# Optimization experiments

Hardware: AMD Instinct MI355X
Metric: run time of the kernel (lower is better)

The kernel has to match this reference:

```python
import jax, jax.numpy as jnp
import numpy as np

E = 1024
H = 16
DH = E // H
EPS = 1e-8
GRAM_W = 1.5


def _gram_scores(q, k1, k2):
    # q: [BH, L, D], k1/k2: [BH, S, D] -> [BH, L, S]
    ll = jnp.sum(q * q, -1)[:, :, None]          # [BH, L, 1]
    vv = jnp.sum(k1 * k1, -1)[:, None, :]        # [BH, 1, S]
    aa = jnp.sum(k2 * k2, -1)[:, None, :]
    va = jnp.sum(k1 * k2, -1)[:, None, :]
    lv = jnp.einsum('bld,bsd->bls', q, k1)
    la = jnp.einsum('bld,bsd->bls', q, k2)
    det = ll * (vv * aa - va * va) - lv * (lv * aa - la * va) + la * (lv * va - la * vv)
    return -jnp.sqrt(jnp.clip(det, EPS, None))


def setup_inputs() -> dict:
    key = jax.random.key(0)
    ks = jax.random.split(key, 20)
    L, B, S = 512, 4, 1024
    inp = {
        'query': jax.random.normal(ks[0], (L, B, E), jnp.float32),
        'mod1': jax.random.normal(ks[1], (S, B, E), jnp.float32),
        'mod2': jax.random.normal(ks[2], (S, B, E), jnp.float32),
    }
    # Linear params stored as [in, out] (y = x @ W + b), 8 linears
    names = ['q', 'k1', 'k2', 'v1', 'v2', 'g1', 'g2', 'o']
    for i, n in enumerate(names):
        inp[n + '_w'] = jax.random.normal(ks[3 + 2 * i], (E, E), jnp.float32) * 0.02
        inp[n + '_b'] = jax.random.normal(ks[4 + 2 * i], (E,), jnp.float32) * 0.02
    return inp


def reference(query, mod1, mod2,
              q_w, q_b, k1_w, k1_b, k2_w, k2_b, v1_w, v1_b, v2_w, v2_b,
              g1_w, g1_b, g2_w, g2_b, o_w, o_b):
    L, B, _ = query.shape
    S = mod1.shape[0]
    scaling = DH ** -0.5

    def lin(x, w, b):
        return x @ w + b

    def split_heads(x, n):  # [n, B, E] -> [B*H, n, DH]
        return x.reshape(n, B * H, DH).transpose(1, 0, 2)

    q = split_heads(lin(query, q_w, q_b) * scaling, L)
    k1 = split_heads(lin(mod1, k1_w, k1_b), S)
    k2 = split_heads(lin(mod2, k2_w, k2_b), S)
    v1 = split_heads(lin(mod1, v1_w, v1_b), S)
    v2 = split_heads(lin(mod2, v2_w, v2_b), S)

    w1 = jnp.einsum('bld,bsd->bls', q, k1)
    w2 = jnp.einsum('bld,bsd->bls', q, k2)
    gram = _gram_scores(q, k1, k2)
    logits = GRAM_W * gram + w1 + w2          # [BH, L, S]
    attn = jax.nn.softmax(logits, axis=-1)

    def merge_heads(x):  # [B*H, L, DH] -> [L, B, E]
        return x.transpose(1, 0, 2).reshape(L, B, E)

    out1 = merge_heads(jnp.einsum('bls,bsd->bld', attn, v1))
    out2 = merge_heads(jnp.einsum('bls,bsd->bld', attn, v2))
    gate1 = jax.nn.sigmoid(lin(query, g1_w, g1_b))
    gate2 = jax.nn.sigmoid(lin(query, g2_w, g2_b))
    attn_output = lin((out1 * gate1 + out2 * gate2) / 2.0, o_w, o_b)
    avg_weights = attn.reshape(B, H, L, S).mean(axis=1)
    return attn_output, avg_weights
```

## Files before the change

kernel.cpp:

```cpp
#include <hip/hip_runtime.h>
#include <cstddef>
#include <cstdint>

typedef unsigned short ushort_t;
typedef unsigned int uint_t;
typedef __attribute__((ext_vector_type(8))) short short8;
typedef __attribute__((ext_vector_type(4))) float f32x4;

#define EDIM 1024
#define NHEAD 16
#define HDIM 64
#define NB 4
#define LQ 512
#define SK 1024
#define BHD 64

__device__ __forceinline__ ushort_t f2b(float f) {
    uint_t u = __float_as_uint(f);
    return (ushort_t)((u + 0x7fffu + ((u >> 16) & 1u)) >> 16);
}
__device__ __forceinline__ float b2f(ushort_t b) {
    return __uint_as_float(((uint_t)b) << 16);
}

__device__ __forceinline__ void gload_lds16(const void* g, void* l) {
    __builtin_amdgcn_global_load_lds((const __attribute__((address_space(1))) void*)g,
                                     (__attribute__((address_space(3))) void*)l, 16, 0, 0);
}

struct MegaArgs {
    const ushort_t *qx, *m1h, *m1l, *m2h, *m2l;
    const ushort_t *Wqg, *Wkv1, *Wkv2, *Wk1l, *Wk2l;
    const float *q_b, *k1_b, *k2_b, *v1_b, *v2_b, *g1_b, *g2_b;
    float *K1f, *K2f;
    ushort_t *V1b, *V2b, *Qb, *G1b, *G2b;
};

__global__ __launch_bounds__(256, 2)
void mega_gemm(MegaArgs a)
{
    __shared__ ushort_t As[128 * 64];
    __shared__ ushort_t Bs[128 * 64];
    const int tid = threadIdx.x;
    const int wave = tid >> 6, lane = tid & 63;
    const int ln = lane & 15, lq = lane >> 4;
    const int wm = wave & 1, wn = wave >> 1;
    const int mrl = lane >> 3;
    const int lswz = (lane & 7) ^ mrl;

    const int id = blockIdx.x;
    f32x4 zero = {0.f, 0.f, 0.f, 0.f};

    if (id < 512) {
        const int kind = id >> 8;
        const int t = id & 255;
        const int u = t >> 3;
        const int col0 = (u >> 2) * 128;
        const int row0 = ((t & 7) * 4 + (u & 3)) * 128;
        const ushort_t* Ah  = kind ? a.m2h : a.m1h;
        const ushort_t* Alo = kind ? a.m2l : a.m1l;
        const ushort_t* Bh  = kind ? a.Wkv2 : a.Wkv1;
        const ushort_t* Blo = kind ? a.Wk2l : a.Wk1l;
        const float* bias = kind ? a.k2_b : a.k1_b;

        f32x4 acc[4][4];
#pragma unroll
        for (int i = 0; i < 4; ++i)
#pragma unroll
            for (int j = 0; j < 4; ++j) acc[i][j] = zero;

        const int ksub = (lswz & 3) * 8;
        const ushort_t* Asrc = (lswz & 4) ? Alo : Ah;
        const ushort_t* Bsrc = (lswz & 4) ? Blo : Bh;

        for (int kk = 0; kk < 1024; kk += 32) {
            __syncthreads();
#pragma unroll
            for (int j = 0; j < 4; ++j) {
                const int mr = (wave * 4 + j) * 8 + mrl;
                gload_lds16(Asrc + (size_t)(row0 + mr) * 1024 + kk + ksub,
                            (void*)(As + (wave * 4 + j) * 512));
                gload_lds16(Bsrc + (size_t)(col0 + mr) * 1024 + kk + ksub,
                            (void*)(Bs + (wave * 4 + j) * 512));
            }
            __syncthreads();
            short8 ah[4], alv[4], bh[4], blv[4];
#pragma unroll
            for (int i = 0; i < 4; ++i) {
                const int ml = wm * 64 + i * 16 + ln;
                const int pa = (lq ^ (ml & 7)) * 8;
                ah[i]  = *(const short8*)(As + ml * 64 + pa);
                alv[i] = *(const short8*)(As + ml * 64 + (pa ^ 32));
                const int nl = wn * 64 + i * 16 + ln;
                const int pb = (lq ^ (nl & 7)) * 8;
                bh[i]  = *(const short8*)(Bs + nl * 64 + pb);
                blv[i] = *(const short8*)(Bs + nl * 64 + (pb ^ 32));
            }
#pragma unroll
            for (int i = 0; i < 4; ++i)
#pragma unroll
                for (int j = 0; j < 4; ++j)
                    acc[i][j] = __builtin_amdgcn_mfma_f32_16x16x32_bf16(ah[i], bh[j], acc[i][j], 0, 0, 0);
#pragma unroll
            for (int i = 0; i < 4; ++i)
#pragma unroll
                for (int j = 0; j < 4; ++j)
                    acc[i][j] = __builtin_amdgcn_mfma_f32_16x16x32_bf16(ah[i], blv[j], acc[i][j], 0, 0, 0);
#pragma unroll
            for (int i = 0; i < 4; ++i)
#pragma unroll
                for (int j = 0; j < 4; ++j)
                    acc[i][j] = __builtin_amdgcn_mfma_f32_16x16x32_bf16(alv[i], bh[j], acc[i][j], 0, 0, 0);
        }

        float* Y = kind ? a.K2f : a.K1f;
#pragma unroll
        for (int i = 0; i < 4; ++i) {
#pragma unroll
            for (int r = 0; r < 4; ++r) {
                const int row = row0 + wm * 64 + i * 16 + lq * 4 + r;
#pragma unroll
                for (int j = 0; j < 4; ++j) {
                    const int col = col0 + wn * 64 + j * 16 + ln;
                    const float v = acc[i][j][r] + bias[col];
                    const int s = row >> 2, b = row & 3, h = col >> 6, d = col & 63;
                    Y[(((size_t)(b * 16 + h)) * 1024 + s) * 64 + d] = v;
                }
            }
        }
        return;
    }

    int kind, row0, col0;
    const ushort_t *A, *B;
    const float* bias;
    if (id < 1024) {
        int t = id - 512; kind = 2 + (t >> 8); t &= 255;
        const int u = t >> 3;
        col0 = (u >> 2) * 128;
        row0 = ((t & 7) * 4 + (u & 3)) * 128;
        A = (kind == 2) ? a.m1h : a.m2h;
        B = ((kind == 2) ? a.Wkv1 : a.Wkv2) + (size_t)1024 * 1024;
        bias = (kind == 2) ? a.v1_b : a.v2_b;
    } else {
        const int t = id - 1024; kind = 4;
        const int u = t >> 3;
        const int c = (t & 7) * 3 + (u >> 4);
        const int rr = u & 15;
        col0 = c * 128; row0 = rr * 128;
        A = a.qx; B = a.Wqg;
        const int seg = c >> 3;
        bias = (seg == 0) ? a.q_b : ((seg == 1) ? a.g1_b : a.g2_b);
    }

    f32x4 acc[4][4];
#pragma unroll
    for (int i = 0; i < 4; ++i)
#pragma unroll
        for (int j = 0; j < 4; ++j) acc[i][j] = zero;

    for (int kk = 0; kk < 1024; kk += 64) {
        __syncthreads();
#pragma unroll
        for (int j = 0; j < 4; ++j) {
            const int mr = (wave * 4 + j) * 8 + mrl;
            gload_lds16(A + (size_t)(row0 + mr) * 1024 + kk + lswz * 8,
                        (void*)(As + (wave * 4 + j) * 512));
            gload_lds16(B + (size_t)(col0 + mr) * 1024 + kk + lswz * 8,
                        (void*)(Bs + (wave * 4 + j) * 512));
        }
        __syncthreads();
#pragma unroll
        for (int sub = 0; sub < 2; ++sub) {
            short8 af[4], bfv[4];
#pragma unroll
            for (int i = 0; i < 4; ++i) {
                const int ml = wm * 64 + i * 16 + ln;
                af[i] = *(const short8*)(As + ml * 64 + (((sub * 4 + lq) ^ (ml & 7)) * 8));
                const int nl = wn * 64 + i * 16 + ln;
                bfv[i] = *(const short8*)(Bs + nl * 64 + (((sub * 4 + lq) ^ (nl & 7)) * 8));
            }
#pragma unroll
            for (int i = 0; i < 4; ++i)
#pragma unroll
                for (int j = 0; j < 4; ++j)
                    acc[i][j] = __builtin_amdgcn_mfma_f32_16x16x32_bf16(af[i], bfv[j], acc[i][j], 0, 0, 0);
        }
    }

#pragma unroll
    for (int i = 0; i < 4; ++i) {
#pragma unroll
        for (int r = 0; r < 4; ++r) {
            const int row = row0 + wm * 64 + i * 16 + lq * 4 + r;
#pragma unroll
            for (int j = 0; j < 4; ++j) {
                const int col = col0 + wn * 64 + j * 16 + ln;
                const int lc = col & 1023;
                float v = acc[i][j][r] + bias[lc];
                if (kind <= 3) {
                    const int s = row >> 2, b = row & 3, h = lc >> 6, d = lc & 63;
                    ushort_t* Y = (kind == 2) ? a.V1b : a.V2b;
                    Y[(((size_t)(b * 16 + h)) * 1024 + s) * 64 + d] = f2b(v);
                } else {
                    const int seg = col >> 10;
                    if (seg == 0) {
                        v *= 0.125f;
                        const int s = row >> 2, b = row & 3, h = lc >> 6, d = lc & 63;
                        a.Qb[(((size_t)(b * 16 + h)) * 512 + s) * 64 + d] = f2b(v);
                    } else {
                        v = 1.0f / (1.0f + __expf(-v));
                        ushort_t* Y = (seg == 1) ? a.G1b : a.G2b;
                        Y[(size_t)row * 1024 + lc] = f2b(v);
                    }
                }
            }
        }
    }
}

struct CastArgs {
    const float* q; const float* m1; const float* m2;
    ushort_t* qx; ushort_t* m1h; ushort_t* m1l; ushort_t* m2h; ushort_t* m2l;
    const float* wsrc[8];
    ushort_t* whi[8];
    ushort_t* wlo[8];
};

__global__ __launch_bounds__(256)
void casts_kernel(CastArgs a)
{
    __shared__ float T[64][65];
    const int id = blockIdx.x;
    const int tid = threadIdx.x;
    if (id < 1024) {
        const size_t i = ((size_t)id * 256 + tid) * 8;
        float4 x = *(const float4*)(a.q + i);
        float4 y = *(const float4*)(a.q + i + 4);
        ushort_t o[8] = {f2b(x.x), f2b(x.y), f2b(x.z), f2b(x.w), f2b(y.x), f2b(y.y), f2b(y.z), f2b(y.w)};
        *(uint4*)( (void*)(a.qx + i) ) = *(const uint4*)o;
    } else if (id < 5120) {
        const int t = id - 1024;
        const int which = t >> 11;
        const float* x = which ? a.m2 : a.m1;
        ushort_t* yh = which ? a.m2h : a.m1h;
        ushort_t* yl = which ? a.m2l : a.m1l;
        const size_t i = ((size_t)(t & 2047) * 256 + tid) * 8;
        float v[8];
        *(float4*)v = *(const float4*)(x + i);
        *(float4*)(v + 4) = *(const float4*)(x + i + 4);
        ushort_t oh[8], ol[8];
#pragma unroll
        for (int k = 0; k < 8; ++k) {
            oh[k] = f2b(v[k]);
            ol[k] = f2b(v[k] - b2f(oh[k]));
        }
        *(uint4*)( (void*)(yh + i) ) = *(const uint4*)oh;
        *(uint4*)( (void*)(yl + i) ) = *(const uint4*)ol;
    } else {
        const int t = id - 5120;
        const int z = t >> 8, x = t & 15, y = (t >> 4) & 15;
        const float* W = a.wsrc[z];
        ushort_t* Th = a.whi[z];
        ushort_t* Tl = a.wlo[z];
        const int k0 = x * 64, n0 = y * 64;
        const int r = tid >> 2, cg = (tid & 3) * 16;
#pragma unroll
        for (int u = 0; u < 4; ++u) {
            float4 v = *(const float4*)(W + (size_t)(k0 + r) * 1024 + n0 + cg + u * 4);
            T[r][cg + u * 4 + 0] = v.x; T[r][cg + u * 4 + 1] = v.y;
            T[r][cg + u * 4 + 2] = v.z; T[r][cg + u * 4 + 3] = v.w;
        }
        __syncthreads();
        ushort_t oh[16], ol[16];
#pragma unroll
        for (int u = 0; u < 16; ++u) {
            float v = T[cg + u][r];
            oh[u] = f2b(v);
            ol[u] = f2b(v - b2f(oh[u]));
        }
        ushort_t* dh = Th + (size_t)(n0 + r) * 1024 + k0 + cg;
        *(uint4*)( (void*)dh ) = *(const uint4*)oh;
        *(uint4*)( (void*)(dh + 8) ) = *(const uint4*)(oh + 8);
        if (Tl) {
            ushort_t* dl = Tl + (size_t)(n0 + r) * 1024 + k0 + cg;
            *(uint4*)( (void*)dl ) = *(const uint4*)ol;
            *(uint4*)( (void*)(dl + 8) ) = *(const uint4*)(ol + 8);
        }
    }
}

__global__ __launch_bounds__(256)
void prep_kernel(const float* __restrict__ K1f, const float* __restrict__ K2f,
                 ushort_t* __restrict__ K1b, ushort_t* __restrict__ K2b,
                 float* __restrict__ vv, float* __restrict__ aa, float* __restrict__ va,
                 const ushort_t* __restrict__ Qb, float* __restrict__ ll,
                 const ushort_t* __restrict__ V1b, const ushort_t* __restrict__ V2b,
                 ushort_t* __restrict__ V1t, ushort_t* __restrict__ V2t)
{
    __shared__ float T[64][65];
    const int id = blockIdx.x;
    const int tid = threadIdx.x;
    const int wave = tid >> 6, lane = tid & 63;
    if (id < 16384) {
        const int row = id * 4 + wave;
        const float x1 = K1f[(size_t)row * 64 + lane];
        const float x2 = K2f[(size_t)row * 64 + lane];
        K1b[(size_t)row * 64 + lane] = f2b(x1);
        K2b[(size_t)row * 64 + lane] = f2b(x2);
        float s1 = x1 * x1, s2 = x2 * x2, s3 = x1 * x2;
#pragma unroll
        for (int o = 1; o < 64; o <<= 1) {
            s1 += __shfl_xor(s1, o);
            s2 += __shfl_xor(s2, o);
            s3 += __shfl_xor(s3, o);
        }
        if (lane == 0) { vv[row] = s1; aa[row] = s2; va[row] = s3; }
    } else if (id < 24576) {
        const int row = (id - 16384) * 4 + wave;
        const float x = b2f(Qb[(size_t)row * 64 + lane]);
        float s = x * x;
#pragma unroll
        for (int o = 1; o < 64; o <<= 1) s += __shfl_xor(s, o);
        if (lane == 0) ll[row] = s;
    } else {
        const int t = id - 24576;
        const int z = t >> 10, bh = (t >> 4) & 63, s0 = (t & 15) * 64;
        const ushort_t* S = z ? V2b : V1b;
        ushort_t* D = z ? V2t : V1t;
        const int r = tid >> 2, cg = (tid & 3) * 16;
        ushort_t buf[16];
        const ushort_t* sp = S + ((size_t)bh * 1024 + s0 + r) * 64 + cg;
        *(uint4*)buf = *(const uint4*)sp;
        *(uint4*)(buf + 8) = *(const uint4*)(sp + 8);
#pragma unroll
        for (int u = 0; u < 16; ++u) T[r][cg + u] = b2f(buf[u]);
        __syncthreads();
        ushort_t o[16];
#pragma unroll
        for (int u = 0; u < 16; ++u) o[u] = f2b(T[cg + u][r]);
        ushort_t* d = D + ((size_t)bh * 64 + r) * 1024 + s0 + cg;
        *(uint4*)( (void*)d ) = *(const uint4*)o;
        *(uint4*)( (void*)(d + 8) ) = *(const uint4*)(o + 8);
    }
}

__global__ __launch_bounds__(256, 2)
void scores_kernel(const ushort_t* __restrict__ Qb, const ushort_t* __restrict__ K1b,
                   const ushort_t* __restrict__ K2b, const float* __restrict__ ll,
                   const float* __restrict__ vv, const float* __restrict__ aa,
                   const float* __restrict__ va, float* __restrict__ logits)
{
    __shared__ ushort_t Qs[128 * 64];
    __shared__ ushort_t K1s[128 * 64];
    __shared__ ushort_t K2s[128 * 64];
    __shared__ float llS[128], vvS[128], aaS[128], vaS[128];
    const int tid = threadIdx.x;
    const int wave = tid >> 6, lane = tid & 63;
    const int ln = lane & 15, lq = lane >> 4;
    const int wm = wave & 1, wn = wave >> 1;
    const int bh = blockIdx.z;
    const int l0 = blockIdx.y * 128, s0 = blockIdx.x * 128;
    const int cswz = (lane & 7) ^ ((lane >> 3) & 7);
    const int mrl = lane >> 3;

    if (tid < 128) {
        llS[tid] = ll[(size_t)bh * 512 + l0 + tid];
        vvS[tid] = vv[(size_t)bh * 1024 + s0 + tid];
        aaS[tid] = aa[(size_t)bh * 1024 + s0 + tid];
        vaS[tid] = va[(size_t)bh * 1024 + s0 + tid];
    }
#pragma unroll
    for (int j = 0; j < 4; ++j) {
        const int mr = (wave * 4 + j) * 8 + mrl;
        gload_lds16(Qb + ((size_t)bh * 512 + l0 + mr) * 64 + cswz * 8, (void*)(Qs + (wave * 4 + j) * 512));
        gload_lds16(K1b + ((size_t)bh * 1024 + s0 + mr) * 64 + cswz * 8, (void*)(K1s + (wave * 4 + j) * 512));
        gload_lds16(K2b + ((size_t)bh * 1024 + s0 + mr) * 64 + cswz * 8, (void*)(K2s + (wave * 4 + j) * 512));
    }
    __syncthreads();

    f32x4 zero = {0.f, 0.f, 0.f, 0.f};
    f32x4 lv[4][4], la[4][4];
#pragma unroll
    for (int i = 0; i < 4; ++i)
#pragma unroll
        for (int j = 0; j < 4; ++j) { lv[i][j] = zero; la[i][j] = zero; }

#pragma unroll
    for (int sub = 0; sub < 2; ++sub) {
        short8 qf[4], k1f[4], k2f[4];
#pragma unroll
        for (int i = 0; i < 4; ++i) {
            const int ml = wm * 64 + i * 16 + ln;
            qf[i] = *(const short8*)(Qs + ml * 64 + (((sub * 4 + lq) ^ (ml & 7)) * 8));
            const int nl = wn * 64 + i * 16 + ln;
            k1f[i] = *(const short8*)(K1s + nl * 64 + (((sub * 4 + lq) ^ (nl & 7)) * 8));
            k2f[i] = *(const short8*)(K2s + nl * 64 + (((sub * 4 + lq) ^ (nl & 7)) * 8));
        }
#pragma unroll
        for (int i = 0; i < 4; ++i)
#pragma unroll
            for (int j = 0; j < 4; ++j) {
                lv[i][j] = __builtin_amdgcn_mfma_f32_16x16x32_bf16(qf[i], k1f[j], lv[i][j], 0, 0, 0);
                la[i][j] = __builtin_amdgcn_mfma_f32_16x16x32_bf16(qf[i], k2f[j], la[i][j], 0, 0, 0);
            }
    }

#pragma unroll
    for (int i = 0; i < 4; ++i) {
#pragma unroll
        for (int r = 0; r < 4; ++r) {
            const int l_loc = wm * 64 + i * 16 + lq * 4 + r;
            const float LL = llS[l_loc];
#pragma unroll
            for (int j = 0; j < 4; ++j) {
                const int s_loc = wn * 64 + j * 16 + ln;
                const float VV = vvS[s_loc], AA = aaS[s_loc], VA = vaS[s_loc];
                const float LV = lv[i][j][r], LA = la[i][j][r];
                float det = LL * (VV * AA - VA * VA) - LV * (LV * AA - LA * VA) + LA * (LV * VA - LA * VV);
                det = fmaxf(det, 1e-8f);
                logits[((size_t)bh * 512 + l0 + l_loc) * 1024 + s0 + s_loc] = LV + LA - 1.5f * sqrtf(det);
            }
        }
    }
}

__global__ __launch_bounds__(256)
void softmax_avg_kernel(float* __restrict__ logits, float* __restrict__ avg)
{
    __shared__ float part[4][1024];
    const int b = blockIdx.x >> 9, l = blockIdx.x & 511;
    const int wave = threadIdx.x >> 6, lane = threadIdx.x & 63;
    float pacc[16];
#pragma unroll
    for (int u = 0; u < 16; ++u) pacc[u] = 0.f;
#pragma unroll
    for (int jj = 0; jj < 4; ++jj) {
        const int h = wave * 4 + jj;
        float* rowp = logits + (((size_t)(b * 16 + h)) * 512 + l) * 1024;
        float4 v[4];
#pragma unroll
        for (int c = 0; c < 4; ++c) v[c] = *(const float4*)(rowp + c * 256 + lane * 4);
        float m = -3.4e38f;
#pragma unroll
        for (int c = 0; c < 4; ++c) m = fmaxf(m, fmaxf(fmaxf(v[c].x, v[c].y), fmaxf(v[c].z, v[c].w)));
#pragma unroll
        for (int o = 1; o < 64; o <<= 1) m = fmaxf(m, __shfl_xor(m, o));
        float s = 0.f;
#pragma unroll
        for (int c = 0; c < 4; ++c) {
            v[c].x = __expf(v[c].x - m); v[c].y = __expf(v[c].y - m);
            v[c].z = __expf(v[c].z - m); v[c].w = __expf(v[c].w - m);
            s += v[c].x + v[c].y + v[c].z + v[c].w;
        }
#pragma unroll
        for (int o = 1; o < 64; o <<= 1) s += __shfl_xor(s, o);
        const float inv = 1.0f / s;
        ushort_t* arow = (ushort_t*)rowp;
#pragma unroll
        for (int c = 0; c < 4; ++c) {
            const float p0 = v[c].x * inv, p1 = v[c].y * inv, p2 = v[c].z * inv, p3 = v[c].w * inv;
            ushort_t w[4] = {f2b(p0), f2b(p1), f2b(p2), f2b(p3)};
            *(uint2*)( (void*)(arow + c * 256 + lane * 4) ) = *(const uint2*)w;
            pacc[c * 4 + 0] += p0; pacc[c * 4 + 1] += p1;
            pacc[c * 4 + 2] += p2; pacc[c * 4 + 3] += p3;
        }
    }
#pragma unroll
    for (int c = 0; c < 4; ++c) {
        float4 pv = {pacc[c * 4 + 0], pacc[c * 4 + 1], pacc[c * 4 + 2], pacc[c * 4 + 3]};
        *(float4*)(&part[wave][c * 256 + lane * 4]) = pv;
    }
    __syncthreads();
    const int s0 = threadIdx.x * 4;
    float4 a0 = *(const float4*)(&part[0][s0]);
    float4 a1 = *(const float4*)(&part[1][s0]);
    float4 a2 = *(const float4*)(&part[2][s0]);
    float4 a3 = *(const float4*)(&part[3][s0]);
    float4 o;
    o.x = (a0.x + a1.x + a2.x + a3.x) * 0.0625f;
    o.y = (a0.y + a1.y + a2.y + a3.y) * 0.0625f;
    o.z = (a0.z + a1.z + a2.z + a3.z) * 0.0625f;
    o.w = (a0.w + a1.w + a2.w + a3.w) * 0.0625f;
    *(float4*)(avg + ((size_t)(b * 512 + l)) * 1024 + s0) = o;
}

__global__ __launch_bounds__(256, 2)
void pv_gate_kernel(const ushort_t* __restrict__ attn, const ushort_t* __restrict__ V1t,
                    const ushort_t* __restrict__ V2t, const ushort_t* __restrict__ G1,
                    const ushort_t* __restrict__ G2, ushort_t* __restrict__ tmpb)
{
    __shared__ ushort_t Ps[128 * 64];
    __shared__ ushort_t V1s[64 * 64];
    __shared__ ushort_t V2s[64 * 64];
    const int tid = threadIdx.x;
    const int wave = tid >> 6, lane = tid & 63;
    const int ln = lane & 15, lq = lane >> 4;
    const int bh = blockIdx.y;
    const int l0 = blockIdx.x * 128;
    const int cswz = (lane & 7) ^ ((lane >> 3) & 7);
    const int mrl = lane >> 3;
    const int bq = bh >> 4, h = bh & 15;

    f32x4 zero = {0.f, 0.f, 0.f, 0.f};
    f32x4 acc1[2][4], acc2[2][4];
#pragma unroll
    for (int i = 0; i < 2; ++i)
#pragma unroll
        for (int j = 0; j < 4; ++j) { acc1[i][j] = zero; acc2[i][j] = zero; }

    for (int s0 = 0; s0 < 1024; s0 += 64) {
        __syncthreads();
#pragma unroll
        for (int j = 0; j < 4; ++j) {
            const int mr = (wave * 4 + j) * 8 + mrl;
            gload_lds16(attn + ((size_t)bh * 512 + l0 + mr) * 2048 + s0 + cswz * 8,
                        (void*)(Ps + (wave * 4 + j) * 512));
        }
#pragma unroll
        for (int j = 0; j < 2; ++j) {
            const int mv = (wave * 2 + j) * 8 + mrl;
            gload_lds16(V1t + ((size_t)bh * 64 + mv) * 1024 + s0 + cswz * 8,
                        (void*)(V1s + (wave * 2 + j) * 512));
            gload_lds16(V2t + ((size_t)bh * 64 + mv) * 1024 + s0 + cswz * 8,
                        (void*)(V2s + (wave * 2 + j) * 512));
        }
        __syncthreads();
#pragma unroll
        for (int sub = 0; sub < 2; ++sub) {
            short8 af[2], b1f[4], b2f_[4];
#pragma unroll
            for (int i = 0; i < 2; ++i) {
                const int ml = wave * 32 + i * 16 + ln;
                af[i] = *(const short8*)(Ps + ml * 64 + (((sub * 4 + lq) ^ (ml & 7)) * 8));
            }
#pragma unroll
            for (int j = 0; j < 4; ++j) {
                const int nl = j * 16 + ln;
                b1f[j] = *(const short8*)(V1s + nl * 64 + (((sub * 4 + lq) ^ (nl & 7)) * 8));
                b2f_[j] = *(const short8*)(V2s + nl * 64 + (((sub * 4 + lq) ^ (nl & 7)) * 8));
            }
#pragma unroll
            for (int i = 0; i < 2; ++i)
#pragma unroll
                for (int j = 0; j < 4; ++j) {
                    acc1[i][j] = __builtin_amdgcn_mfma_f32_16x16x32_bf16(af[i], b1f[j], acc1[i][j], 0, 0, 0);
                    acc2[i][j] = __builtin_amdgcn_mfma_f32_16x16x32_bf16(af[i], b2f_[j], acc2[i][j], 0, 0, 0);
                }
        }
    }

#pragma unroll
    for (int i = 0; i < 2; ++i) {
#pragma unroll
        for (int r = 0; r < 4; ++r) {
            const int l = l0 + wave * 32 + i * 16 + lq * 4 + r;
#pragma unroll
            for (int j = 0; j < 4; ++j) {
                const int d = j * 16 + ln;
                const size_t addr = ((size_t)l * 4 + bq) * 1024 + h * 64 + d;
                const float v = 0.5f * (acc1[i][j][r] * b2f(G1[addr]) + acc2[i][j][r] * b2f(G2[addr]));
                tmpb[addr] = f2b(v);
            }
        }
    }
}

__global__ __launch_bounds__(256, 2)
void gemm_o64(const ushort_t* __restrict__ A, const ushort_t* __restrict__ B,
              const float* __restrict__ bias, float* __restrict__ Y)
{
    __shared__ ushort_t As[64 * 64];
    __shared__ ushort_t Bs[128 * 64];
    const int tid = threadIdx.x;
    const int wave = tid >> 6, lane = tid & 63;
    const int ln = lane & 15, lq = lane >> 4;
    const int row0 = blockIdx.y * 64, col0 = blockIdx.x * 128;
    const int wm = wave & 1, wn = wave >> 1;
    const int cswz = (lane & 7) ^ ((lane >> 3) & 7);
    const int mrl = lane >> 3;

    f32x4 zero = {0.f, 0.f, 0.f, 0.f};
    f32x4 acc[2][4];
#pragma unroll
    for (int i = 0; i < 2; ++i)
#pragma unroll
        for (int j = 0; j < 4; ++j) acc[i][j] = zero;

    for (int kk = 0; kk < 1024; kk += 64) {
        __syncthreads();
#pragma unroll
        for (int j = 0; j < 2; ++j) {
            const int mr = (wave * 2 + j) * 8 + mrl;
            gload_lds16(A + (size_t)(row0 + mr) * 1024 + kk + cswz * 8,
                        (void*)(As + (wave * 2 + j) * 512));
        }
#pragma unroll
        for (int j = 0; j < 4; ++j) {
            const int mr = (wave * 4 + j) * 8 + mrl;
            gload_lds16(B + (size_t)(col0 + mr) * 1024 + kk + cswz * 8,
                        (void*)(Bs + (wave * 4 + j) * 512));
        }
        __syncthreads();
#pragma unroll
        for (int sub = 0; sub < 2; ++sub) {
            short8 af[2], bfv[4];
#pragma unroll
            for (int i = 0; i < 2; ++i) {
                const int ml = wm * 32 + i * 16 + ln;
                af[i] = *(const short8*)(As + ml * 64 + (((sub * 4 + lq) ^ (ml & 7)) * 8));
            }
#pragma unroll
            for (int j = 0; j < 4; ++j) {
                const int nl = wn * 64 + j * 16 + ln;
                bfv[j] = *(const short8*)(Bs + nl * 64 + (((sub * 4 + lq) ^ (nl & 7)) * 8));
            }
#pragma unroll
            for (int i = 0; i < 2; ++i)
#pragma unroll
                for (int j = 0; j < 4; ++j)
                    acc[i][j] = __builtin_amdgcn_mfma_f32_16x16x32_bf16(af[i], bfv[j], acc[i][j], 0, 0, 0);
        }
    }

#pragma unroll
    for (int i = 0; i < 2; ++i) {
#pragma unroll
        for (int r = 0; r < 4; ++r) {
            const int row = row0 + wm * 32 + i * 16 + lq * 4 + r;
#pragma unroll
            for (int j = 0; j < 4; ++j) {
                const int col = col0 + wn * 64 + j * 16 + ln;
                Y[(size_t)row * 1024 + col] = acc[i][j][r] + bias[col];
            }
        }
    }
}

extern "C" void kernel_launch(void* const* d_in, const int* in_sizes, int n_in,
                              void* d_out, int out_size, void* d_ws, size_t ws_size,
                              hipStream_t stream)
{
    const float* query = (const float*)d_in[0];
    const float* mod1  = (const float*)d_in[1];
    const float* mod2  = (const float*)d_in[2];
    const float* q_w  = (const float*)d_in[3];  const float* q_b  = (const float*)d_in[4];
    const float* k1_w = (const float*)d_in[5];  const float* k1_b = (const float*)d_in[6];
    const float* k2_w = (const float*)d_in[7];  const float* k2_b = (const float*)d_in[8];
    const float* v1_w = (const float*)d_in[9];  const float* v1_b = (const float*)d_in[10];
    const float* v2_w = (const float*)d_in[11]; const float* v2_b = (const float*)d_in[12];
    const float* g1_w = (const float*)d_in[13]; const float* g1_b = (const float*)d_in[14];
    const float* g2_w = (const float*)d_in[15]; const float* g2_b = (const float*)d_in[16];
    const float* o_w  = (const float*)d_in[17]; const float* o_b  = (const float*)d_in[18];
    float* out = (float*)d_out;

    const size_t MB = 1u << 20;
    char* w = (char*)d_ws;
    ushort_t* Wqg  = (ushort_t*)(w + 0 * MB);
    ushort_t* Wkv1 = (ushort_t*)(w + 6 * MB);
    ushort_t* Wkv2 = (ushort_t*)(w + 10 * MB);
    ushort_t* Wo   = (ushort_t*)(w + 14 * MB);
    ushort_t* Wk1l = (ushort_t*)(w + 16 * MB);
    ushort_t* Wk2l = (ushort_t*)(w + 18 * MB);
    ushort_t* qx   = (ushort_t*)(w + 20 * MB);
    ushort_t* tmpb = qx;
    ushort_t* Qb   = (ushort_t*)(w + 24 * MB);
    ushort_t* K1b  = (ushort_t*)(w + 28 * MB);
    ushort_t* K2b  = (ushort_t*)(w + 36 * MB);
    ushort_t* V1t  = (ushort_t*)(w + 44 * MB);
    ushort_t* V2t  = (ushort_t*)(w + 52 * MB);
    ushort_t* G1b  = (ushort_t*)(w + 60 * MB);
    ushort_t* G2b  = (ushort_t*)(w + 64 * MB);
    float* ll = (float*)(w + 68 * MB);
    float* vv = (float*)(w + 68 * MB + 256 * 1024);
    float* aa = (float*)(w + 68 * MB + 512 * 1024);
    float* va = (float*)(w + 68 * MB + 768 * 1024);
    float* logits = (float*)(w + 78 * MB);
    ushort_t* m1h = (ushort_t*)(w + 78 * MB);
    ushort_t* m2h = (ushort_t*)(w + 86 * MB);
    ushort_t* m1l = (ushort_t*)(w + 94 * MB);
    ushort_t* m2l = (ushort_t*)(w + 102 * MB);
    float* K1f = (float*)(w + 110 * MB);
    float* K2f = (float*)(w + 126 * MB);
    ushort_t* V1b = (ushort_t*)(w + 142 * MB);
    ushort_t* V2b = (ushort_t*)(w + 150 * MB);
    ushort_t* attn = (ushort_t*)logits;

    CastArgs ca;
    ca.q = query; ca.m1 = mod1; ca.m2 = mod2;
    ca.qx = qx; ca.m1h = m1h; ca.m1l = m1l; ca.m2h = m2h; ca.m2l = m2l;
    const float* srcs[8] = {q_w, g1_w, g2_w, k1_w, v1_w, k2_w, v2_w, o_w};
    ushort_t* his[8] = {Wqg, Wqg + (size_t)1024 * 1024, Wqg + (size_t)2048 * 1024,
                        Wkv1, Wkv1 + (size_t)1024 * 1024, Wkv2, Wkv2 + (size_t)1024 * 1024, Wo};
    ushort_t* los[8] = {nullptr, nullptr, nullptr, Wk1l, nullptr, Wk2l, nullptr, nullptr};
    for (int i = 0; i < 8; ++i) { ca.wsrc[i] = srcs[i]; ca.whi[i] = his[i]; ca.wlo[i] = los[i]; }
    casts_kernel<<<7168, 256, 0, stream>>>(ca);

    MegaArgs ma;
    ma.qx = qx; ma.m1h = m1h; ma.m1l = m1l; ma.m2h = m2h; ma.m2l = m2l;
    ma.Wqg = Wqg; ma.Wkv1 = Wkv1; ma.Wkv2 = Wkv2; ma.Wk1l = Wk1l; ma.Wk2l = Wk2l;
    ma.q_b = q_b; ma.k1_b = k1_b; ma.k2_b = k2_b; ma.v1_b = v1_b; ma.v2_b = v2_b;
    ma.g1_b = g1_b; ma.g2_b = g2_b;
    ma.K1f = K1f; ma.K2f = K2f; ma.V1b = V1b; ma.V2b = V2b;
    ma.Qb = Qb; ma.G1b = G1b; ma.G2b = G2b;
    mega_gemm<<<1408, 256, 0, stream>>>(ma);

    prep_kernel<<<26624, 256, 0, stream>>>(K1f, K2f, K1b, K2b, vv, aa, va,
                                           Qb, ll, V1b, V2b, V1t, V2t);

    scores_kernel<<<dim3(8, 4, 64), 256, 0, stream>>>(Qb, K1b, K2b, ll, vv, aa, va, logits);
    softmax_avg_kernel<<<2048, 256, 0, stream>>>(logits, out + (size_t)LQ * NB * EDIM);
    pv_gate_kernel<<<dim3(4, 64), 256, 0, stream>>>(attn, V1t, V2t, G1b, G2b, tmpb);
    gemm_o64<<<dim3(8, 32), 256, 0, stream>>>(tmpb, Wo, o_b, out);
}
```

Before: 372.0 us.

## Fuse scores and softmax into two-pass recompute kernel writing bf16 probabilities

```diff
diff --git a/kernel.cpp b/kernel.cpp
--- a/kernel.cpp
+++ b/kernel.cpp
@@ -293,7 +293,8 @@
 __global__ __launch_bounds__(256)
 void prep_kernel(const float* __restrict__ K1f, const float* __restrict__ K2f,
                  ushort_t* __restrict__ K1b, ushort_t* __restrict__ K2b,
-                 float* __restrict__ vv, float* __restrict__ aa, float* __restrict__ va,
+                 float* __restrict__ vv, float* __restrict__ aa,
+                 float* __restrict__ va2, float* __restrict__ gg,
                  const ushort_t* __restrict__ Qb, float* __restrict__ ll,
                  const ushort_t* __restrict__ V1b, const ushort_t* __restrict__ V2b,
                  ushort_t* __restrict__ V1t, ushort_t* __restrict__ V2t)
@@ -315,7 +316,11 @@
             s2 += __shfl_xor(s2, o);
             s3 += __shfl_xor(s3, o);
         }
-        if (lane == 0) { vv[row] = s1; aa[row] = s2; va[row] = s3; }
+        if (lane == 0) {
+            vv[row] = s1; aa[row] = s2;
+            va2[row] = 2.0f * s3;
+            gg[row] = s1 * s2 - s3 * s3;
+        }
     } else if (id < 24576) {
         const int row = (id - 16384) * 4 + wave;
         const float x = b2f(Qb[(size_t)row * 64 + lane]);
@@ -346,158 +351,173 @@
 }
 
 __global__ __launch_bounds__(256, 2)
-void scores_kernel(const ushort_t* __restrict__ Qb, const ushort_t* __restrict__ K1b,
-                   const ushort_t* __restrict__ K2b, const float* __restrict__ ll,
-                   const float* __restrict__ vv, const float* __restrict__ aa,
-                   const float* __restrict__ va, float* __restrict__ logits)
+void attn_fused(const ushort_t* __restrict__ Qb, const ushort_t* __restrict__ K1b,
+                const ushort_t* __restrict__ K2b, const float* __restrict__ ll,
+                const float* __restrict__ vv, const float* __restrict__ aa,
+                const float* __restrict__ va2, const float* __restrict__ gg,
+                ushort_t* __restrict__ attn)
 {
-    __shared__ ushort_t Qs[128 * 64];
+    __shared__ ushort_t Qs[64 * 64];
     __shared__ ushort_t K1s[128 * 64];
     __shared__ ushort_t K2s[128 * 64];
-    __shared__ float llS[128], vvS[128], aaS[128], vaS[128];
+    __shared__ float vvS[1024], aaS[1024], vaS[1024], ggS[1024], llS[64];
     const int tid = threadIdx.x;
     const int wave = tid >> 6, lane = tid & 63;
     const int ln = lane & 15, lq = lane >> 4;
-    const int wm = wave & 1, wn = wave >> 1;
-    const int bh = blockIdx.z;
-    const int l0 = blockIdx.y * 128, s0 = blockIdx.x * 128;
-    const int cswz = (lane & 7) ^ ((lane >> 3) & 7);
     const int mrl = lane >> 3;
-
-    if (tid < 128) {
-        llS[tid] = ll[(size_t)bh * 512 + l0 + tid];
-        vvS[tid] = vv[(size_t)bh * 1024 + s0 + tid];
-        aaS[tid] = aa[(size_t)bh * 1024 + s0 + tid];
-        vaS[tid] = va[(size_t)bh * 1024 + s0 + tid];
-    }
-#pragma unroll
-    for (int j = 0; j < 4; ++j) {
-        const int mr = (wave * 4 + j) * 8 + mrl;
-        gload_lds16(Qb + ((size_t)bh * 512 + l0 + mr) * 64 + cswz * 8, (void*)(Qs + (wave * 4 + j) * 512));
-        gload_lds16(K1b + ((size_t)bh * 1024 + s0 + mr) * 64 + cswz * 8, (void*)(K1s + (wave * 4 + j) * 512));
-        gload_lds16(K2b + ((size_t)bh * 1024 + s0 + mr) * 64 + cswz * 8, (void*)(K2s + (wave * 4 + j) * 512));
-    }
-    __syncthreads();
-
-    f32x4 zero = {0.f, 0.f, 0.f, 0.f};
-    f32x4 lv[4][4], la[4][4];
-#pragma unroll
-    for (int i = 0; i < 4; ++i)
-#pragma unroll
-        for (int j = 0; j < 4; ++j) { lv[i][j] = zero; la[i][j] = zero; }
-
-#pragma unroll
-    for (int sub = 0; sub < 2; ++sub) {
-        short8 qf[4], k1f[4], k2f[4];
-#pragma unroll
-        for (int i = 0; i < 4; ++i) {
-            const int ml = wm * 64 + i * 16 + ln;
-            qf[i] = *(const short8*)(Qs + ml * 64 + (((sub * 4 + lq) ^ (ml & 7)) * 8));
-            const int nl = wn * 64 + i * 16 + ln;
-            k1f[i] = *(const short8*)(K1s + nl * 64 + (((sub * 4 + lq) ^ (nl & 7)) * 8));
-            k2f[i] = *(const short8*)(K2s + nl * 64 + (((sub * 4 + lq) ^ (nl & 7)) * 8));
-        }
-#pragma unroll
-        for (int i = 0; i < 4; ++i)
-#pragma unroll
-            for (int j = 0; j < 4; ++j) {
-                lv[i][j] = __builtin_amdgcn_mfma_f32_16x16x32_bf16(qf[i], k1f[j], lv[i][j], 0, 0, 0);
-                la[i][j] = __builtin_amdgcn_mfma_f32_16x16x32_bf16(qf[i], k2f[j], la[i][j], 0, 0, 0);
-            }
-    }
-
-#pragma unroll
-    for (int i = 0; i < 4; ++i) {
+    const int cswz = (lane & 7) ^ mrl;
+
+    const int id = blockIdx.x;
+    const int bh = (id & 7) * 8 + ((id >> 3) & 7);
+    const int l0 = (id >> 6) * 64;
+
+    for (int i = tid; i < 1024; i += 256) {
+        vvS[i] = vv[(size_t)bh * 1024 + i];
+        aaS[i] = aa[(size_t)bh * 1024 + i];
+        vaS[i] = va2[(size_t)bh * 1024 + i];
+        ggS[i] = gg[(size_t)bh * 1024 + i];
+    }
+    if (tid < 64) llS[tid] = ll[(size_t)bh * 512 + l0 + tid];
+#pragma unroll
+    for (int j = 0; j < 2; ++j) {
+        const int mr = (wave * 2 + j) * 8 + mrl;
+        gload_lds16(Qb + ((size_t)bh * 512 + l0 + mr) * 64 + cswz * 8,
+                    (void*)(Qs + (wave * 2 + j) * 512));
+    }
+
+    const int ml = wave * 16 + ln;
+
+    auto tile_logits = [&](int s0, float lgt[8][4]) {
+        __syncthreads();
+#pragma unroll
+        for (int j = 0; j < 4; ++j) {
+            const int mr = (wave * 4 + j) * 8 + mrl;
+            gload_lds16(K1b + ((size_t)bh * 1024 + s0 + mr) * 64 + cswz * 8,
+                        (void*)(K1s + (wave * 4 + j) * 512));
+            gload_lds16(K2b + ((size_t)bh * 1024 + s0 + mr) * 64 + cswz * 8,
+                        (void*)(K2s + (wave * 4 + j) * 512));
+        }
+        __syncthreads();
+        f32x4 zero = {0.f, 0.f, 0.f, 0.f};
+        f32x4 lv[8], la[8];
+#pragma unroll
+        for (int j = 0; j < 8; ++j) { lv[j] = zero; la[j] = zero; }
+#pragma unroll
+        for (int sub = 0; sub < 2; ++sub) {
+            const short8 qf = *(const short8*)(Qs + ml * 64 + (((sub * 4 + lq) ^ (ml & 7)) * 8));
+#pragma unroll
+            for (int j = 0; j < 8; ++j) {
+                const int nl = j * 16 + ln;
+                const short8 k1f = *(const short8*)(K1s + nl * 64 + (((sub * 4 + lq) ^ (nl & 7)) * 8));
+                const short8 k2f = *(const short8*)(K2s + nl * 64 + (((sub * 4 + lq) ^ (nl & 7)) * 8));
+                lv[j] = __builtin_amdgcn_mfma_f32_16x16x32_bf16(qf, k1f, lv[j], 0, 0, 0);
+                la[j] = __builtin_amdgcn_mfma_f32_16x16x32_bf16(qf, k2f, la[j], 0, 0, 0);
+            }
+        }
+#pragma unroll
+        for (int j = 0; j < 8; ++j) {
+            const int c = s0 + j * 16 + ln;
+            const float VV = vvS[c], AA = aaS[c], VA2 = vaS[c], GB = ggS[c];
+#pragma unroll
+            for (int r = 0; r < 4; ++r) {
+                const float LL = llS[wave * 16 + lq * 4 + r];
+                const float LV = lv[j][r], LA = la[j][r];
+                float det = LL * GB;
+                det = fmaf(-AA, LV * LV, det);
+                det = fmaf(VA2, LV * LA, det);
+                det = fmaf(-VV, LA * LA, det);
+                det = fmaxf(det, 1e-8f);
+                lgt[j][r] = (LV + LA) - 1.5f * sqrtf(det);
+            }
+        }
+    };
+
+    float m_run[4], s_run[4];
+#pragma unroll
+    for (int r = 0; r < 4; ++r) { m_run[r] = -3.0e38f; s_run[r] = 0.f; }
+
+    for (int s0 = 0; s0 < 1024; s0 += 128) {
+        float lgt[8][4];
+        tile_logits(s0, lgt);
+        float tmax[4];
+#pragma unroll
+        for (int r = 0; r < 4; ++r) tmax[r] = -3.0e38f;
+#pragma unroll
+        for (int j = 0; j < 8; ++j)
+#pragma unroll
+            for (int r = 0; r < 4; ++r) tmax[r] = fmaxf(tmax[r], lgt[j][r]);
 #pragma unroll
         for (int r = 0; r < 4; ++r) {
-            const int l_loc = wm * 64 + i * 16 + lq * 4 + r;
-            const float LL = llS[l_loc];
-#pragma unroll
-            for (int j = 0; j < 4; ++j) {
-                const int s_loc = wn * 64 + j * 16 + ln;
-                const float VV = vvS[s_loc], AA = aaS[s_loc], VA = vaS[s_loc];
-                const float LV = lv[i][j][r], LA = la[i][j][r];
-                float det = LL * (VV * AA - VA * VA) - LV * (LV * AA - LA * VA) + LA * (LV * VA - LA * VV);
-                det = fmaxf(det, 1e-8f);
-                logits[((size_t)bh * 512 + l0 + l_loc) * 1024 + s0 + s_loc] = LV + LA - 1.5f * sqrtf(det);
-            }
-        }
-    }
-}
-
-__global__ __launch_bounds__(256)
-void softmax_avg_kernel(float* __restrict__ logits, float* __restrict__ avg)
-{
-    __shared__ float part[4][1024];
-    const int b = blockIdx.x >> 9, l = blockIdx.x & 511;
-    const int wave = threadIdx.x >> 6, lane = threadIdx.x & 63;
-    float pacc[16];
-#pragma unroll
-    for (int u = 0; u < 16; ++u) pacc[u] = 0.f;
-#pragma unroll
-    for (int jj = 0; jj < 4; ++jj) {
-        const int h = wave * 4 + jj;
-        float* rowp = logits + (((size_t)(b * 16 + h)) * 512 + l) * 1024;
-        float4 v[4];
-#pragma unroll
-        for (int c = 0; c < 4; ++c) v[c] = *(const float4*)(rowp + c * 256 + lane * 4);
-        float m = -3.4e38f;
-#pragma unroll
-        for (int c = 0; c < 4; ++c) m = fmaxf(m, fmaxf(fmaxf(v[c].x, v[c].y), fmaxf(v[c].z, v[c].w)));
-#pragma unroll
-        for (int o = 1; o < 64; o <<= 1) m = fmaxf(m, __shfl_xor(m, o));
-        float s = 0.f;
-#pragma unroll
-        for (int c = 0; c < 4; ++c) {
-            v[c].x = __expf(v[c].x - m); v[c].y = __expf(v[c].y - m);
-            v[c].z = __expf(v[c].z - m); v[c].w = __expf(v[c].w - m);
-            s += v[c].x + v[c].y + v[c].z + v[c].w;
-        }
-#pragma unroll
-        for (int o = 1; o < 64; o <<= 1) s += __shfl_xor(s, o);
-        const float inv = 1.0f / s;
-        ushort_t* arow = (ushort_t*)rowp;
-#pragma unroll
-        for (int c = 0; c < 4; ++c) {
-            const float p0 = v[c].x * inv, p1 = v[c].y * inv, p2 = v[c].z * inv, p3 = v[c].w * inv;
-            ushort_t w[4] = {f2b(p0), f2b(p1), f2b(p2), f2b(p3)};
-            *(uint2*)( (void*)(arow + c * 256 + lane * 4) ) = *(const uint2*)w;
-            pacc[c * 4 + 0] += p0; pacc[c * 4 + 1] += p1;
-            pacc[c * 4 + 2] += p2; pacc[c * 4 + 3] += p3;
-        }
-    }
-#pragma unroll
-    for (int c = 0; c < 4; ++c) {
-        float4 pv = {pacc[c * 4 + 0], pacc[c * 4 + 1], pacc[c * 4 + 2], pacc[c * 4 + 3]};
-        *(float4*)(&part[wave][c * 256 + lane * 4]) = pv;
-    }
-    __syncthreads();
-    const int s0 = threadIdx.x * 4;
-    float4 a0 = *(const float4*)(&part[0][s0]);
-    float4 a1 = *(const float4*)(&part[1][s0]);
-    float4 a2 = *(const float4*)(&part[2][s0]);
-    float4 a3 = *(const float4*)(&part[3][s0]);
-    float4 o;
-    o.x = (a0.x + a1.x + a2.x + a3.x) * 0.0625f;
-    o.y = (a0.y + a1.y + a2.y + a3.y) * 0.0625f;
-    o.z = (a0.z + a1.z + a2.z + a3.z) * 0.0625f;
-    o.w = (a0.w + a1.w + a2.w + a3.w) * 0.0625f;
-    *(float4*)(avg + ((size_t)(b * 512 + l)) * 1024 + s0) = o;
+#pragma unroll
+            for (int o = 1; o < 16; o <<= 1) tmax[r] = fmaxf(tmax[r], __shfl_xor(tmax[r], o));
+        }
+#pragma unroll
+        for (int r = 0; r < 4; ++r) {
+            const float mn = fmaxf(m_run[r], tmax[r]);
+            const float sc = __expf(m_run[r] - mn);
+            float ps = 0.f;
+#pragma unroll
+            for (int j = 0; j < 8; ++j) ps += __expf(lgt[j][r] - mn);
+            s_run[r] = s_run[r] * sc + ps;
+            m_run[r] = mn;
+        }
+    }
+    float inv[4];
+#pragma unroll
+    for (int r = 0; r < 4; ++r) {
+        float s = s_run[r];
+#pragma unroll
+        for (int o = 1; o < 16; o <<= 1) s += __shfl_xor(s, o);
+        inv[r] = 1.0f / s;
+    }
+
+    for (int s0 = 0; s0 < 1024; s0 += 128) {
+        float lgt[8][4];
+        tile_logits(s0, lgt);
+#pragma unroll
+        for (int j = 0; j < 8; ++j) {
+            const int c = s0 + j * 16 + ln;
+#pragma unroll
+            for (int r = 0; r < 4; ++r) {
+                const float p = __expf(lgt[j][r] - m_run[r]) * inv[r];
+                attn[((size_t)bh * 512 + l0 + wave * 16 + lq * 4 + r) * 1024 + c] = f2b(p);
+            }
+        }
+    }
 }
 
 __global__ __launch_bounds__(256, 2)
 void pv_gate_kernel(const ushort_t* __restrict__ attn, const ushort_t* __restrict__ V1t,
                     const ushort_t* __restrict__ V2t, const ushort_t* __restrict__ G1,
-                    const ushort_t* __restrict__ G2, ushort_t* __restrict__ tmpb)
+                    const ushort_t* __restrict__ G2, ushort_t* __restrict__ tmpb,
+                    float* __restrict__ avg)
 {
     __shared__ ushort_t Ps[128 * 64];
     __shared__ ushort_t V1s[64 * 64];
     __shared__ ushort_t V2s[64 * 64];
     const int tid = threadIdx.x;
+
+    if (blockIdx.x >= 256) {
+        const int t = blockIdx.x - 256;
+        const int b = t >> 9, l = t & 511;
+        const int c0 = tid * 4;
+        float s0_ = 0.f, s1_ = 0.f, s2_ = 0.f, s3_ = 0.f;
+#pragma unroll
+        for (int h = 0; h < 16; ++h) {
+            const ushort_t* p = attn + (((size_t)(b * 16 + h)) * 512 + l) * 1024 + c0;
+            ushort_t u[4];
+            *(uint2*)u = *(const uint2*)p;
+            s0_ += b2f(u[0]); s1_ += b2f(u[1]); s2_ += b2f(u[2]); s3_ += b2f(u[3]);
+        }
+        float4 o = {s0_ * 0.0625f, s1_ * 0.0625f, s2_ * 0.0625f, s3_ * 0.0625f};
+        *(float4*)(avg + ((size_t)(b * 512 + l)) * 1024 + c0) = o;
+        return;
+    }
+
     const int wave = tid >> 6, lane = tid & 63;
     const int ln = lane & 15, lq = lane >> 4;
-    const int bh = blockIdx.y;
-    const int l0 = blockIdx.x * 128;
+    const int bh = blockIdx.x >> 2;
+    const int l0 = (blockIdx.x & 3) * 128;
     const int cswz = (lane & 7) ^ ((lane >> 3) & 7);
     const int mrl = lane >> 3;
     const int bq = bh >> 4, h = bh & 15;
@@ -514,7 +534,7 @@
 #pragma unroll
         for (int j = 0; j < 4; ++j) {
             const int mr = (wave * 4 + j) * 8 + mrl;
-            gload_lds16(attn + ((size_t)bh * 512 + l0 + mr) * 2048 + s0 + cswz * 8,
+            gload_lds16(attn + ((size_t)bh * 512 + l0 + mr) * 1024 + s0 + cswz * 8,
                         (void*)(Ps + (wave * 4 + j) * 512));
         }
 #pragma unroll
@@ -671,11 +691,12 @@
     ushort_t* V2t  = (ushort_t*)(w + 52 * MB);
     ushort_t* G1b  = (ushort_t*)(w + 60 * MB);
     ushort_t* G2b  = (ushort_t*)(w + 64 * MB);
-    float* ll = (float*)(w + 68 * MB);
-    float* vv = (float*)(w + 68 * MB + 256 * 1024);
-    float* aa = (float*)(w + 68 * MB + 512 * 1024);
-    float* va = (float*)(w + 68 * MB + 768 * 1024);
-    float* logits = (float*)(w + 78 * MB);
+    float* ll  = (float*)(w + 68 * MB);
+    float* vv  = (float*)(w + 68 * MB + 256 * 1024);
+    float* aa  = (float*)(w + 68 * MB + 512 * 1024);
+    float* va2 = (float*)(w + 68 * MB + 768 * 1024);
+    float* gg  = (float*)(w + 68 * MB + 1024 * 1024);
+    ushort_t* attn = (ushort_t*)(w + 78 * MB);
     ushort_t* m1h = (ushort_t*)(w + 78 * MB);
     ushort_t* m2h = (ushort_t*)(w + 86 * MB);
     ushort_t* m1l = (ushort_t*)(w + 94 * MB);
@@ -684,7 +705,6 @@
     float* K2f = (float*)(w + 126 * MB);
     ushort_t* V1b = (ushort_t*)(w + 142 * MB);
     ushort_t* V2b = (ushort_t*)(w + 150 * MB);
-    ushort_t* attn = (ushort_t*)logits;
 
     CastArgs ca;
     ca.q = query; ca.m1 = mod1; ca.m2 = mod2;
@@ -705,11 +725,13 @@
     ma.Qb = Qb; ma.G1b = G1b; ma.G2b = G2b;
     mega_gemm<<<1408, 256, 0, stream>>>(ma);
 
-    prep_kernel<<<26624, 256, 0, stream>>>(K1f, K2f, K1b, K2b, vv, aa, va,
+    prep_kernel<<<26624, 256, 0, stream>>>(K1f, K2f, K1b, K2b, vv, aa, va2, gg,
                                            Qb, ll, V1b, V2b, V1t, V2t);
 
-    scores_kernel<<<dim3(8, 4, 64), 256, 0, stream>>>(Qb, K1b, K2b, ll, vv, aa, va, logits);
-    softmax_avg_kernel<<<2048, 256, 0, stream>>>(logits, out + (size_t)LQ * NB * EDIM);
-    pv_gate_kernel<<<dim3(4, 64), 256, 0, stream>>>(attn, V1t, V2t, G1b, G2b, tmpb);
+    attn_fused<<<512, 256, 0, stream>>>(Qb, K1b, K2b, ll, vv, aa, va2, gg, attn);
+
+    pv_gate_kernel<<<2304, 256, 0, stream>>>(attn, V1t, V2t, G1b, G2b, tmpb,
+                                             out + (size_t)LQ * NB * EDIM);
+
     gemm_o64<<<dim3(8, 32), 256, 0, stream>>>(tmpb, Wo, o_b, out);
 }
```

Result: slower. 387.4 us (+4.2%).
